# Kernel optimization log

Measured on AMD Instinct MI355X. Metric: run time of the kernel, lower is better.

## Reference

```python
import jax, jax.numpy as jnp
import numpy as np
from jax import lax

B, N, C, T = 8, 2000, 32, 12
K, F_CHEV, F_TIME = 3, 64, 64
LN_EPS = 1e-5


def setup_inputs() -> dict:
    key = jax.random.key(0)
    ks = jax.random.split(key, 20)
    s = 0.1
    return {
        "x": jax.random.normal(ks[0], (B, N, C, T), jnp.float32),
        "cheb_polys": jax.random.normal(ks[1], (K, N, N), jnp.float32) * 0.02,
        # temporal attention params
        "U1": jax.random.normal(ks[2], (N,), jnp.float32) * s,
        "U2": jax.random.normal(ks[3], (C, N), jnp.float32) * s,
        "U3": jax.random.normal(ks[4], (C,), jnp.float32) * s,
        "be": jax.random.normal(ks[5], (1, T, T), jnp.float32) * s,
        "Ve": jax.random.normal(ks[6], (T, T), jnp.float32) * s,
        # spatial attention params
        "W1": jax.random.normal(ks[7], (T,), jnp.float32) * s,
        "W2": jax.random.normal(ks[8], (C, T), jnp.float32) * s,
        "W3": jax.random.normal(ks[9], (C,), jnp.float32) * s,
        "bs": jax.random.normal(ks[10], (1, N, N), jnp.float32) * s,
        "Vs": jax.random.normal(ks[11], (N, N), jnp.float32) * (s / np.sqrt(N)),
        # Chebyshev conv params, stacked (K, C, F_chev)
        "Theta": jax.random.normal(ks[12], (K, C, F_CHEV), jnp.float32) * (1.0 / np.sqrt(C)),
        # time conv (1x3) and residual conv (1x1), NCHW/OIHW layout
        "tc_w": jax.random.normal(ks[13], (F_TIME, F_CHEV, 1, 3), jnp.float32) * (1.0 / np.sqrt(3 * F_CHEV)),
        "tc_b": jnp.zeros((F_TIME,), jnp.float32),
        "rc_w": jax.random.normal(ks[14], (F_TIME, C, 1, 1), jnp.float32) * (1.0 / np.sqrt(C)),
        "rc_b": jnp.zeros((F_TIME,), jnp.float32),
        # LayerNorm over nb_time_filter
        "ln_g": jnp.ones((F_TIME,), jnp.float32),
        "ln_b": jnp.zeros((F_TIME,), jnp.float32),
    }


def _conv2d(x, w, b, stride_t):
    # x: (B, Cin, N, T), w: (Cout, Cin, kh, kw)
    pad_w = (w.shape[3] - 1) // 2
    y = lax.conv_general_dilated(
        x, w, window_strides=(1, stride_t),
        padding=[(0, 0), (pad_w, pad_w)],
        dimension_numbers=("NCHW", "OIHW", "NCHW"))
    return y + b[None, :, None, None]


def reference(x, cheb_polys, U1, U2, U3, be, Ve, W1, W2, W3, bs, Vs,
              Theta, tc_w, tc_b, rc_w, rc_b, ln_g, ln_b):
    b, n, c, t = x.shape

    # ---- temporal attention: (B, T, T) ----
    lhs = jnp.einsum("bnct,n->btc", x, U1)              # x.permute(0,3,2,1) @ U1
    lhs = jnp.einsum("btc,cn->btn", lhs, U2)
    rhs = jnp.einsum("c,bnct->bnt", U3, x)
    E = jnp.einsum("ij,bjk->bik", Ve,
                   jax.nn.sigmoid(jnp.einsum("btn,bnu->btu", lhs, rhs) + be))
    temporal_At = jax.nn.softmax(E, axis=1)             # (B, T, T)

    # apply temporal attention
    x_TAt = jnp.matmul(x.reshape(b, n * c, t), temporal_At).reshape(b, n, c, t)

    # ---- spatial attention on x_TAt: (B, N, N) ----
    lhs_s = jnp.einsum("bnct,t->bnc", x_TAt, W1)
    lhs_s = jnp.einsum("bnc,ct->bnt", lhs_s, W2)
    rhs_s = jnp.einsum("c,bnct->btn", W3, x_TAt)        # (W3 @ x).transpose(-1,-2)
    S = jnp.einsum("ij,bjk->bik", Vs,
                   jax.nn.sigmoid(jnp.einsum("bnt,btm->bnm", lhs_s, rhs_s) + bs))
    spatial_At = jax.nn.softmax(S, axis=1)              # (B, N, N)

    # ---- Chebyshev graph conv with spatial attention ----
    # A[b,k,j,i] = cheb[k,j,i] * SAt[b,j,i]; out = relu(sum_k A^T x Theta_k)
    A = cheb_polys[None, :, :, :] * spatial_At[:, None, :, :]   # (B, K, N, N)
    h = jnp.einsum("bkji,bjct->bkitc", A, x)                    # (B, K, N, T, C)
    spatial_gcn = jax.nn.relu(jnp.einsum("bkitc,kcf->bift", h, Theta))  # (B, N, F, T)

    # ---- temporal conv + residual + LayerNorm ----
    time_out = _conv2d(spatial_gcn.transpose(0, 2, 1, 3), tc_w, tc_b, 1)  # (B, F_time, N, T')
    x_res = _conv2d(x.transpose(0, 2, 1, 3), rc_w, rc_b, 1)               # (B, F_time, N, T')
    z = jax.nn.relu(x_res + time_out).transpose(0, 3, 2, 1)               # (B, T', N, F_time)

    mu = jnp.mean(z, axis=-1, keepdims=True)
    var = jnp.mean((z - mu) ** 2, axis=-1, keepdims=True)
    zn = (z - mu) * lax.rsqrt(var + LN_EPS) * ln_g + ln_b

    return zn.transpose(0, 2, 3, 1)                                       # (B, N, F_time, T')
```

## Files before the change

kernel.cpp:

```cpp
#include <hip/hip_runtime.h>
#include <hip/hip_bf16.h>
#include <math.h>

#define B_ 8
#define N_ 2000
#define C_ 32
#define T_ 12
#define K_ 3
#define FC_ 64
#define FT_ 64
#define PW 2048

typedef short bf16x8 __attribute__((ext_vector_type(8)));
typedef float f32x4 __attribute__((ext_vector_type(4)));

__device__ __forceinline__ float sigmoidf(float v) { return 1.0f / (1.0f + __expf(-v)); }
__device__ __forceinline__ float bf2f(unsigned short u) {
    union { unsigned int i; float f; } v; v.i = ((unsigned int)u) << 16; return v.f;
}
__device__ __forceinline__ unsigned short f2bf(float f) {
    union { __hip_bfloat16 h; unsigned short u; } v; v.h = __float2bfloat16(f); return v.u;
}
typedef const __attribute__((address_space(1))) void* gas_t;
typedef __attribute__((address_space(3))) void* las_t;
__device__ __forceinline__ void gload16(const unsigned short* g, unsigned short* l) {
    __builtin_amdgcn_global_load_lds((gas_t)g, (las_t)l, 16, 0, 0);
}

__global__ __launch_bounds__(256) void k_tprep(const float* __restrict__ x, const float* __restrict__ U1,
                                               const float* __restrict__ U3,
                                               float* __restrict__ rhsT, float* __restrict__ plh) {
    int b = blockIdx.y, chunk = blockIdx.x;
    int tid = threadIdx.x;
    int nl = tid >> 5, c = tid & 31;
    int w = tid >> 6;
    float u3 = U3[c];
    float plA[12];
#pragma unroll
    for (int t = 0; t < 12; ++t) plA[t] = 0.f;
    for (int it = 0; it < 5; ++it) {
        int n = chunk * 40 + it * 8 + nl;
        const float* xp = x + ((size_t)(b * 2000 + n) * 32 + c) * 12;
        float4 v0 = *(const float4*)xp, v1 = *(const float4*)(xp + 4), v2 = *(const float4*)(xp + 8);
        float xv[12] = {v0.x, v0.y, v0.z, v0.w, v1.x, v1.y, v1.z, v1.w, v2.x, v2.y, v2.z, v2.w};
        float rv[12];
#pragma unroll
        for (int t = 0; t < 12; ++t) rv[t] = u3 * xv[t];
#pragma unroll
        for (int off = 16; off >= 1; off >>= 1)
#pragma unroll
            for (int t = 0; t < 12; ++t) rv[t] += __shfl_xor(rv[t], off);
        if (c == 0) {
#pragma unroll
            for (int t = 0; t < 12; ++t) rhsT[(size_t)(b * 2000 + n) * 12 + t] = rv[t];
        }
        float u1 = U1[n];
#pragma unroll
        for (int t = 0; t < 12; ++t) plA[t] += u1 * xv[t];
    }
#pragma unroll
    for (int t = 0; t < 12; ++t) plA[t] += __shfl_xor(plA[t], 32);
    __shared__ float accs[4][32][12];
    if ((tid & 63) < 32) {
#pragma unroll
        for (int t = 0; t < 12; ++t) accs[w][c][t] = plA[t];
    }
    __syncthreads();
    if (tid < 384) {
        int c2 = tid / 12, t2 = tid % 12;
        float s = accs[0][c2][t2] + accs[1][c2][t2] + accs[2][c2][t2] + accs[3][c2][t2];
        plh[((size_t)(b * 50 + chunk)) * 384 + tid] = s;
    }
}

__global__ __launch_bounds__(256) void k_tred(const float* __restrict__ plh, float* __restrict__ lhs1) {
    int b = blockIdx.x;
    for (int q = threadIdx.x; q < 384; q += 256) {
        const float* p = plh + (size_t)b * 50 * 384 + q;
        float s = 0.f;
        for (int ch = 0; ch < 50; ++ch) s += p[(size_t)ch * 384];
        int c = q / 12, t = q % 12;
        lhs1[(b * 12 + t) * 32 + c] = s;
    }
}

__global__ __launch_bounds__(256) void k_lhsT(const float* __restrict__ lhs1, const float* __restrict__ U2,
                                              float* __restrict__ lhsT) {
    int gid = blockIdx.x * 256 + threadIdx.x;
    if (gid >= B_ * T_ * N_) return;
    int n = gid % N_;
    int bt = gid / N_;
    const float* l1 = lhs1 + bt * C_;
    float a = 0.f;
#pragma unroll
    for (int c = 0; c < C_; ++c) a += l1[c] * U2[c * N_ + n];
    lhsT[gid] = a;
}

__global__ __launch_bounds__(256) void k_tatt1(const float* __restrict__ lhsT, const float* __restrict__ rhsT,
                                               float* __restrict__ pP) {
    int b = blockIdx.y, ch = blockIdx.x;
    int tid = threadIdx.x;
    int n0 = ch * 125;
    __shared__ float sL[12][128];
    __shared__ float sR[128][12];
    for (int q = tid; q < 12 * 125; q += 256) {
        int t = q / 125, nn = q % 125;
        sL[t][nn] = lhsT[(size_t)(b * 12 + t) * 2000 + n0 + nn];
    }
    for (int q = tid; q < 125 * 12; q += 256) {
        int nn = q / 12, t = q % 12;
        sR[nn][t] = rhsT[(size_t)(b * 2000 + n0 + nn) * 12 + t];
    }
    __syncthreads();
    if (tid < 144) {
        int tP = tid / 12, uP = tid % 12;
        float a = 0.f;
#pragma unroll 5
        for (int nn = 0; nn < 125; ++nn) a += sL[tP][nn] * sR[nn][uP];
        pP[(size_t)(b * 16 + ch) * 144 + tid] = a;
    }
}

__global__ __launch_bounds__(256) void k_tatt2(const float* __restrict__ pP, const float* __restrict__ be,
                                               const float* __restrict__ Ve, float* __restrict__ At) {
    int b = blockIdx.x, tid = threadIdx.x;
    __shared__ float sp[144], sE[144], mk[12], sk[12];
    int tP = tid / 12, uP = tid % 12;
    if (tid < 144) {
        float a = 0.f;
#pragma unroll
        for (int ch = 0; ch < 16; ++ch) a += pP[(size_t)(b * 16 + ch) * 144 + tid];
        sp[tid] = sigmoidf(a + be[tid]);
    }
    __syncthreads();
    if (tid < 144) {
        float e = 0.f;
#pragma unroll
        for (int j = 0; j < 12; ++j) e += Ve[tP * 12 + j] * sp[j * 12 + uP];
        sE[tid] = e;
    }
    __syncthreads();
    if (tid < 12) {
        float m = -1e30f;
#pragma unroll
        for (int i = 0; i < 12; ++i) m = fmaxf(m, sE[i * 12 + tid]);
        float s = 0.f;
#pragma unroll
        for (int i = 0; i < 12; ++i) s += __expf(sE[i * 12 + tid] - m);
        mk[tid] = m; sk[tid] = 1.0f / s;
    }
    __syncthreads();
    if (tid < 144) At[b * 144 + tid] = __expf(sE[tid] - mk[uP]) * sk[uP];
}

__global__ __launch_bounds__(256) void k_xsp(const float* __restrict__ x, const float* __restrict__ At,
                                             const float* __restrict__ W1, const float* __restrict__ W2,
                                             const float* __restrict__ W3,
                                             float* __restrict__ lhs_s, float* __restrict__ rhs_s) {
    int b = blockIdx.y, chunk = blockIdx.x;
    int tid = threadIdx.x, nl = tid >> 5, c = tid & 31;
    int n = chunk * 8 + nl;
    __shared__ float atl[144];
    __shared__ float w2l[384];
    __shared__ float w1l[12];
    if (tid < 144) atl[tid] = At[b * 144 + tid];
    if (tid >= 144 && tid < 156) w1l[tid - 144] = W1[tid - 144];
    for (int q = tid; q < 384; q += 256) w2l[q] = W2[q];
    __syncthreads();
    const float* xp = x + ((size_t)(b * 2000 + n) * 32 + c) * 12;
    float4 v0 = *(const float4*)xp, v1 = *(const float4*)(xp + 4), v2 = *(const float4*)(xp + 8);
    float xv[12] = {v0.x, v0.y, v0.z, v0.w, v1.x, v1.y, v1.z, v1.w, v2.x, v2.y, v2.z, v2.w};
    float xa[12];
#pragma unroll
    for (int t = 0; t < 12; ++t) {
        float s = 0.f;
#pragma unroll
        for (int u = 0; u < 12; ++u) s += xv[u] * atl[u * 12 + t];
        xa[t] = s;
    }
    float w3 = W3[c];
    float rv[12], lv[12];
    float l1 = 0.f;
#pragma unroll
    for (int t = 0; t < 12; ++t) l1 += xa[t] * w1l[t];
#pragma unroll
    for (int t = 0; t < 12; ++t) { rv[t] = w3 * xa[t]; lv[t] = l1 * w2l[c * 12 + t]; }
#pragma unroll
    for (int off = 16; off >= 1; off >>= 1)
#pragma unroll
        for (int t = 0; t < 12; ++t) { rv[t] += __shfl_xor(rv[t], off); lv[t] += __shfl_xor(lv[t], off); }
    if (c == 0) {
#pragma unroll
        for (int t = 0; t < 12; ++t) rhs_s[(size_t)(b * 12 + t) * 2000 + n] = rv[t];
#pragma unroll
        for (int t = 0; t < 12; ++t) lhs_s[(size_t)(b * 2000 + n) * 12 + t] = lv[t];
    }
}

__global__ __launch_bounds__(256) void k_wprep(const float* __restrict__ tc_w, const float* __restrict__ rc_w,
                                               float* __restrict__ tcwT, float* __restrict__ rcwT) {
    int gid = blockIdx.x * 256 + threadIdx.x;
    if (gid < 12288) {
        int fi = gid / 192, rem = gid % 192, f = rem / 3, d = rem % 3;
        tcwT[gid] = tc_w[(f * 64 + fi) * 3 + d];
    } else if (gid < 14336) {
        int q = gid - 12288;
        int c = q >> 6, f = q & 63;
        rcwT[q] = rc_w[f * 32 + c];
    }
}

__global__ __launch_bounds__(256) void k_vsb(const float* __restrict__ Vs, unsigned short* __restrict__ Vsb) {
    int gid = blockIdx.x * 256 + threadIdx.x;
    int row = gid >> 8, chunk = gid & 255;
    int p0 = chunk * 8;
    unsigned short o[8];
#pragma unroll
    for (int e = 0; e < 8; ++e) {
        int p = p0 + e;
        o[e] = (row < N_ && p < N_) ? f2bf(Vs[row * N_ + p]) : (unsigned short)0;
    }
    *(int4*)(Vsb + (size_t)row * PW + p0) = *(int4*)o;
}

__global__ __launch_bounds__(256) void k_chebT(const float* __restrict__ cheb, unsigned short* __restrict__ chebT) {
    int j0 = blockIdx.x * 64, i0 = blockIdx.y * 64, kk = blockIdx.z;
    __shared__ float Tl[64][65];
    int t = threadIdx.x;
    int rr = t >> 2, c0 = (t & 3) * 16;
    int j = j0 + rr;
#pragma unroll
    for (int e = 0; e < 16; ++e) {
        int i = i0 + c0 + e;
        Tl[rr][c0 + e] = (j < N_ && i < N_) ? cheb[(size_t)kk * 4000000 + (size_t)j * N_ + i] : 0.f;
    }
    __syncthreads();
    int l = t & 63, w = t >> 6;
    unsigned short o[16];
#pragma unroll
    for (int e = 0; e < 16; ++e) o[e] = f2bf(Tl[w * 16 + e][l]);
    unsigned short* dst = chebT + (size_t)kk * PW * PW + (size_t)(i0 + l) * PW + j0 + w * 16;
    *(int4*)dst = *(int4*)o;
    *(int4*)(dst + 8) = *(int4*)(o + 8);
}

__global__ __launch_bounds__(256) void k_xT(const float* __restrict__ x, unsigned short* __restrict__ xT) {
    int j0 = blockIdx.x * 64, r0 = blockIdx.y * 64, b = blockIdx.z;
    __shared__ float Tl[64][65];
    int t = threadIdx.x;
    int rr = t >> 2, c0 = (t & 3) * 16;
    int j = j0 + rr;
#pragma unroll
    for (int e = 0; e < 16; ++e) {
        int r = r0 + c0 + e;
        Tl[rr][c0 + e] = (j < N_) ? x[(size_t)(b * N_ + j) * 384 + r] : 0.f;
    }
    __syncthreads();
    int l = t & 63, w = t >> 6;
    unsigned short o[16];
#pragma unroll
    for (int e = 0; e < 16; ++e) o[e] = f2bf(Tl[w * 16 + e][l]);
    unsigned short* dst = xT + (size_t)b * 384 * PW + (size_t)(r0 + l) * PW + j0 + w * 16;
    *(int4*)dst = *(int4*)o;
    *(int4*)(dst + 8) = *(int4*)(o + 8);
}

__global__ __launch_bounds__(256) void k_sig(const float* __restrict__ lhs_s, const float* __restrict__ rhs_s,
                                             const float* __restrict__ bs, unsigned short* __restrict__ sigT) {
    int p0 = blockIdx.x * 64, i0 = blockIdx.y * 64, b = blockIdx.z;
    __shared__ float sL[64][12];
    __shared__ float sR[12][64];
    __shared__ float bsl[64][65];
    int t = threadIdx.x;
    for (int q = t; q < 768; q += 256) {
        int pp = q / 12, tt = q % 12;
        int p = p0 + pp;
        sL[pp][tt] = (p < N_) ? lhs_s[(b * N_ + p) * 12 + tt] : 0.f;
    }
    for (int q = t; q < 768; q += 256) {
        int tt = q >> 6, ii = q & 63;
        int i = i0 + ii;
        sR[tt][ii] = (i < N_) ? rhs_s[b * (T_ * N_) + tt * N_ + i] : 0.f;
    }
    {
        int pp = t >> 2, c0 = (t & 3) * 16;
        int p = p0 + pp;
        if (p < N_ && i0 + c0 + 15 < N_) {
            const float* src = bs + (size_t)p * N_ + i0 + c0;
#pragma unroll
            for (int e = 0; e < 16; e += 4) *(float4*)&bsl[pp][c0 + e] = *(const float4*)(src + e);
        } else {
#pragma unroll
            for (int e = 0; e < 16; ++e) {
                int i = i0 + c0 + e;
                bsl[pp][c0 + e] = (p < N_ && i < N_) ? bs[(size_t)p * N_ + i] : 0.f;
            }
        }
    }
    __syncthreads();
    int ii = t & 63, w = t >> 6;
    int i = i0 + ii;
    unsigned short o[16];
#pragma unroll
    for (int e = 0; e < 16; ++e) {
        int pl = w * 16 + e;
        int p = p0 + pl;
        float v = 0.f;
        if (p < N_ && i < N_) {
            float d = bsl[pl][ii];
#pragma unroll
            for (int tt = 0; tt < 12; ++tt) d += sL[pl][tt] * sR[tt][ii];
            v = sigmoidf(d);
        }
        o[e] = f2bf(v);
    }
    unsigned short* dst = sigT + (size_t)b * PW * PW + (size_t)i * PW + p0 + w * 16;
    *(int4*)dst = *(int4*)o;
    *(int4*)(dst + 8) = *(int4*)(o + 8);
}

__global__ __launch_bounds__(512) void k_gemm_S_mfma(const unsigned short* __restrict__ Vsb,
                                                     const unsigned short* __restrict__ sigT,
                                                     unsigned short* __restrict__ ST) {
    int lid = blockIdx.x + (blockIdx.y << 3) + (blockIdx.z << 6);
    int swz = (lid & 7) * 64 + (lid >> 3);
    int j0 = (swz & 7) * 256;
    int i0 = ((swz >> 3) & 7) * 256;
    int b = swz >> 6;
    const unsigned short* Ap = sigT + (size_t)b * PW * PW;
    __shared__ unsigned short As[4][8192];
    __shared__ unsigned short Bs[4][8192];
    int t = threadIdx.x, lane = t & 63, w = t >> 6;
    int wr = w >> 2, wc = w & 3;
    f32x4 acc[8][4];
#pragma unroll
    for (int m = 0; m < 8; ++m)
#pragma unroll
        for (int n = 0; n < 4; ++n)
#pragma unroll
            for (int q = 0; q < 4; ++q) acc[m][n][q] = 0.f;
    int srow = t >> 2;
    int sseg = (t & 3) ^ (srow & 3);
    const unsigned short* gA = Ap + (size_t)(i0 + srow) * PW + sseg * 8;
    const unsigned short* gB = Vsb + (size_t)(j0 + srow) * PW + sseg * 8;
    int ldw = w * 512;
#define STG(slot, kt) do { \
    gload16(gA + (size_t)(kt) * 32, &As[slot][ldw]); \
    gload16(gA + (size_t)128 * PW + (size_t)(kt) * 32, &As[slot][4096 + ldw]); \
    gload16(gB + (size_t)(kt) * 32, &Bs[slot][ldw]); \
    gload16(gB + (size_t)128 * PW + (size_t)(kt) * 32, &Bs[slot][4096 + ldw]); \
} while (0)
    STG(0, 0); STG(1, 1); STG(2, 2);
    int l15 = lane & 15;
    int swr = ((lane >> 4) ^ (lane & 3)) * 8;
    int abase = (wr * 128 + l15) * 32 + swr;
    int bbase = (wc * 64 + l15) * 32 + swr;
    for (int kt = 0; kt < 64; ++kt) {
        if (kt < 62)       asm volatile("s_waitcnt vmcnt(8)" ::: "memory");
        else if (kt == 62) asm volatile("s_waitcnt vmcnt(4)" ::: "memory");
        else               asm volatile("s_waitcnt vmcnt(0)" ::: "memory");
        __builtin_amdgcn_s_barrier();
        __builtin_amdgcn_sched_barrier(0);
        if (kt + 3 < 64) STG((kt + 3) & 3, kt + 3);
        int slot = kt & 3;
        bf16x8 af[8], bfv[4];
#pragma unroll
        for (int m = 0; m < 8; ++m) af[m] = *(const bf16x8*)&As[slot][abase + m * 512];
#pragma unroll
        for (int n = 0; n < 4; ++n) bfv[n] = *(const bf16x8*)&Bs[slot][bbase + n * 512];
        __builtin_amdgcn_s_setprio(1);
#pragma unroll
        for (int m = 0; m < 8; ++m)
#pragma unroll
            for (int n = 0; n < 4; ++n)
                acc[m][n] = __builtin_amdgcn_mfma_f32_16x16x32_bf16(af[m], bfv[n], acc[m][n], 0, 0, 0);
        __builtin_amdgcn_s_setprio(0);
    }
#undef STG
    unsigned short* Sp = ST + (size_t)b * PW * PW;
#pragma unroll
    for (int m = 0; m < 8; ++m) {
        int row0 = i0 + wr * 128 + m * 16 + ((lane >> 4) << 2);
#pragma unroll
        for (int n = 0; n < 4; ++n) {
            int col = j0 + wc * 64 + n * 16 + (lane & 15);
#pragma unroll
            for (int q = 0; q < 4; ++q)
                Sp[(size_t)(row0 + q) * PW + col] = f2bf(acc[m][n][q]);
        }
    }
}

__global__ __launch_bounds__(256) void k_smrow(const unsigned short* __restrict__ ST,
                                               float* __restrict__ gm, float* __restrict__ gs) {
    int wid = threadIdx.x >> 6, lane = threadIdx.x & 63;
    int b = blockIdx.y;
    int i = blockIdx.x * 4 + wid;
    const unsigned short* rp = ST + (size_t)b * PW * PW + (size_t)i * PW;
    float vals[32];
    float m = -1e30f;
#pragma unroll
    for (int k = 0; k < 4; ++k) {
        int j0 = lane * 8 + k * 512;
        if (j0 < N_) {
            union { int4 v; unsigned short s[8]; } u;
            u.v = *(const int4*)(rp + j0);
#pragma unroll
            for (int e = 0; e < 8; ++e) {
                vals[k * 8 + e] = bf2f(u.s[e]);
                m = fmaxf(m, vals[k * 8 + e]);
            }
        } else {
#pragma unroll
            for (int e = 0; e < 8; ++e) vals[k * 8 + e] = -1e30f;
        }
    }
#pragma unroll
    for (int off = 32; off >= 1; off >>= 1) m = fmaxf(m, __shfl_xor(m, off));
    float s = 0.f;
#pragma unroll
    for (int k = 0; k < 32; ++k) s += __expf(vals[k] - m);
#pragma unroll
    for (int off = 32; off >= 1; off >>= 1) s += __shfl_xor(s, off);
    if (lane == 0) {
        gm[b * 2048 + i] = m;
        gs[b * 2048 + i] = 1.0f / s;
    }
}

__global__ __launch_bounds__(512) void k_gemm_cheb_mfma(const unsigned short* __restrict__ chebT,
                                                        const unsigned short* __restrict__ ST,
                                                        const float* __restrict__ gm, const float* __restrict__ gs,
                                                        const unsigned short* __restrict__ xT,
                                                        unsigned short* __restrict__ h2) {
    int bk = blockIdx.y;
    int b = bk / 3, kk = bk % 3;
    int i0 = blockIdx.x * 128;
    const unsigned short* Ac = chebT + (size_t)kk * PW * PW;
    const unsigned short* Sa = ST + (size_t)b * PW * PW;
    const unsigned short* Bx = xT + (size_t)b * 384 * PW;
    __shared__ unsigned short As[2][4096];
    __shared__ unsigned short Bs[2][12288];
    int t = threadIdx.x, lane = t & 63, w = t >> 6;
    int wr = w >> 2, wc = w & 3;
    f32x4 acc[4][6];
#pragma unroll
    for (int a = 0; a < 4; ++a)
#pragma unroll
        for (int c = 0; c < 6; ++c)
#pragma unroll
            for (int q = 0; q < 4; ++q) acc[a][c][q] = 0.f;
    int arow = t >> 2, aq = t & 3;
    const unsigned short* gc = Ac + (size_t)(i0 + arow) * PW + aq * 8;
    const unsigned short* gsat = Sa + (size_t)(i0 + arow) * PW + aq * 8;
    float gmv = gm[b * 2048 + i0 + arow];
    float gsv = gs[b * 2048 + i0 + arow];
    int aoff = arow * 32 + (aq ^ (arow & 3)) * 8;
    int bseg = (t & 3) ^ ((t >> 2) & 3);
    const unsigned short* gB = Bx + (size_t)(t >> 2) * PW + bseg * 8;
    int ldso = w * 512;
#define STAGE_B(buf, p) do { \
    gload16(gB + (p), &Bs[buf][ldso]); \
    gload16(gB + 128 * PW + (p), &Bs[buf][4096 + ldso]); \
    gload16(gB + 256 * PW + (p), &Bs[buf][8192 + ldso]); \
} while (0)
    union U8 { int4 v; unsigned short s[8]; };
    U8 ca, sa;
    ca.v = *(const int4*)gc;
    sa.v = *(const int4*)gsat;
    STAGE_B(0, 0);
    {
        U8 o;
#pragma unroll
        for (int e = 0; e < 8; ++e) o.s[e] = f2bf(bf2f(ca.s[e]) * __expf(bf2f(sa.s[e]) - gmv) * gsv);
        *(int4*)&As[0][aoff] = o.v;
    }
    ca.v = *(const int4*)(gc + 32);
    sa.v = *(const int4*)(gsat + 32);
    __syncthreads();
    int cur = 0;
    int rswz = ((lane >> 4) ^ (lane & 3)) * 8;
    for (int p = 0; p < PW; p += 32) {
        if (p + 32 < PW) {
            STAGE_B(cur ^ 1, p + 32);
            U8 o;
#pragma unroll
            for (int e = 0; e < 8; ++e) o.s[e] = f2bf(bf2f(ca.s[e]) * __expf(bf2f(sa.s[e]) - gmv) * gsv);
            *(int4*)&As[cur ^ 1][aoff] = o.v;
            int pn = (p + 64 < PW) ? p + 64 : 0;
            ca.v = *(const int4*)(gc + pn);
            sa.v = *(const int4*)(gsat + pn);
        }
        bf16x8 af[4], bfr[6];
#pragma unroll
        for (int fm = 0; fm < 4; ++fm)
            af[fm] = *(const bf16x8*)&As[cur][(wr * 64 + fm * 16 + (lane & 15)) * 32 + rswz];
#pragma unroll
        for (int fn = 0; fn < 6; ++fn)
            bfr[fn] = *(const bf16x8*)&Bs[cur][(wc * 96 + fn * 16 + (lane & 15)) * 32 + rswz];
#pragma unroll
        for (int fm = 0; fm < 4; ++fm)
#pragma unroll
            for (int fn = 0; fn < 6; ++fn)
                acc[fm][fn] = __builtin_amdgcn_mfma_f32_16x16x32_bf16(af[fm], bfr[fn], acc[fm][fn], 0, 0, 0);
        __syncthreads();
        cur ^= 1;
    }
#undef STAGE_B
    unsigned short* hp = h2 + (size_t)bk * 768000;
#pragma unroll
    for (int fm = 0; fm < 4; ++fm) {
        int row0 = i0 + wr * 64 + fm * 16 + ((lane >> 4) << 2);
#pragma unroll
        for (int fn = 0; fn < 6; ++fn) {
            int col = wc * 96 + fn * 16 + (lane & 15);
#pragma unroll
            for (int q = 0; q < 4; ++q) {
                int row = row0 + q;
                if (row < N_) hp[(size_t)row * 384 + col] = f2bf(acc[fm][fn][q]);
            }
        }
    }
}

__global__ __launch_bounds__(512) void k_final3(const float* __restrict__ x, const unsigned short* __restrict__ h2,
                                                const float* __restrict__ ThetaG,
                                                const float* __restrict__ tcwT, const float* __restrict__ tc_b,
                                                const float* __restrict__ rcwT, const float* __restrict__ rc_b,
                                                const float* __restrict__ ln_g, const float* __restrict__ ln_b,
                                                float* __restrict__ out) {
    __shared__ __align__(16) char smem[110848];
    unsigned int* gl = (unsigned int*)smem;
    unsigned short* th = (unsigned short*)(smem + 98560);
    float* red_s = (float*)(smem + 98560);
    float* red_q = red_s + 64 * 13;

    int tid = threadIdx.x;
    int n_l = tid & 63, fg = tid >> 6;
    int b = blockIdx.y;
    int node = blockIdx.x * 64 + n_l;
    bool ok = node < N_;
    int nd = ok ? node : N_ - 1;

    for (int q = tid; q < 6144; q += 512) th[q] = f2bf(ThetaG[q]);
    __syncthreads();

    float acc[8][12];
#pragma unroll
    for (int ff = 0; ff < 8; ++ff)
#pragma unroll
        for (int t = 0; t < 12; ++t) acc[ff][t] = 0.f;
    const unsigned short* hb = h2 + (size_t)b * 3 * 768000 + (size_t)nd * 384;
#pragma unroll
    for (int kk = 0; kk < 3; ++kk) {
        const unsigned short* hp = hb + (size_t)kk * 768000;
#pragma unroll 2
        for (int c = 0; c < 32; ++c) {
            const unsigned short* hq = hp + c * 12;
            uint2 u0 = *(const uint2*)(hq);
            uint2 u1 = *(const uint2*)(hq + 4);
            uint2 u2 = *(const uint2*)(hq + 8);
            float h[12];
            h[0] = bf2f((unsigned short)u0.x);  h[1] = bf2f((unsigned short)(u0.x >> 16));
            h[2] = bf2f((unsigned short)u0.y);  h[3] = bf2f((unsigned short)(u0.y >> 16));
            h[4] = bf2f((unsigned short)u1.x);  h[5] = bf2f((unsigned short)(u1.x >> 16));
            h[6] = bf2f((unsigned short)u1.y);  h[7] = bf2f((unsigned short)(u1.y >> 16));
            h[8] = bf2f((unsigned short)u2.x);  h[9] = bf2f((unsigned short)(u2.x >> 16));
            h[10] = bf2f((unsigned short)u2.y); h[11] = bf2f((unsigned short)(u2.y >> 16));
            const unsigned short* wv = th + (kk * 32 + c) * 64 + fg * 8;
            uint2 w01 = *(const uint2*)wv;
            uint2 w23 = *(const uint2*)(wv + 4);
            float wf[8];
            wf[0] = bf2f((unsigned short)w01.x); wf[1] = bf2f((unsigned short)(w01.x >> 16));
            wf[2] = bf2f((unsigned short)w01.y); wf[3] = bf2f((unsigned short)(w01.y >> 16));
            wf[4] = bf2f((unsigned short)w23.x); wf[5] = bf2f((unsigned short)(w23.x >> 16));
            wf[6] = bf2f((unsigned short)w23.y); wf[7] = bf2f((unsigned short)(w23.y >> 16));
#pragma unroll
            for (int ff = 0; ff < 8; ++ff)
#pragma unroll
                for (int t = 0; t < 12; ++t) acc[ff][t] = fmaf(h[t], wf[ff], acc[ff][t]);
        }
    }
    unsigned int* gr = gl + n_l * 385 + fg * 48;
#pragma unroll
    for (int ff = 0; ff < 8; ++ff)
#pragma unroll
        for (int tp = 0; tp < 6; ++tp) {
            float a0 = fmaxf(acc[ff][2 * tp], 0.f), a1 = fmaxf(acc[ff][2 * tp + 1], 0.f);
            gr[ff * 6 + tp] = (unsigned int)f2bf(a0) | ((unsigned int)f2bf(a1) << 16);
        }
    __syncthreads();

    float z[8][12];
#pragma unroll
    for (int ff = 0; ff < 8; ++ff) {
        float bias = tc_b[fg * 8 + ff] + rc_b[fg * 8 + ff];
#pragma unroll
        for (int t = 0; t < 12; ++t) z[ff][t] = bias;
    }
    const float* xp = x + (size_t)(b * 2000 + nd) * 384;
#pragma unroll 2
    for (int c = 0; c < 32; ++c) {
        float4 x0 = *(const float4*)(xp + c * 12);
        float4 x1 = *(const float4*)(xp + c * 12 + 4);
        float4 x2 = *(const float4*)(xp + c * 12 + 8);
        float xv[12] = {x0.x, x0.y, x0.z, x0.w, x1.x, x1.y, x1.z, x1.w, x2.x, x2.y, x2.z, x2.w};
        float4 r0 = *(const float4*)(rcwT + c * 64 + fg * 8);
        float4 r1 = *(const float4*)(rcwT + c * 64 + fg * 8 + 4);
        float rw[8] = {r0.x, r0.y, r0.z, r0.w, r1.x, r1.y, r1.z, r1.w};
#pragma unroll
        for (int ff = 0; ff < 8; ++ff)
#pragma unroll
            for (int t = 0; t < 12; ++t) z[ff][t] = fmaf(xv[t], rw[ff], z[ff][t]);
    }
    const unsigned int* grow = gl + n_l * 385;
    for (int fi = 0; fi < 64; ++fi) {
        float g[12];
#pragma unroll
        for (int j = 0; j < 6; ++j) {
            unsigned int u = grow[fi * 6 + j];
            g[2 * j] = bf2f((unsigned short)u);
            g[2 * j + 1] = bf2f((unsigned short)(u >> 16));
        }
        const float* wp = tcwT + (fi * 64 + fg * 8) * 3;
        float4 w0 = *(const float4*)(wp);
        float4 w1 = *(const float4*)(wp + 4);
        float4 w2 = *(const float4*)(wp + 8);
        float4 w3 = *(const float4*)(wp + 12);
        float4 w4 = *(const float4*)(wp + 16);
        float4 w5 = *(const float4*)(wp + 20);
        float wb[24] = {w0.x, w0.y, w0.z, w0.w, w1.x, w1.y, w1.z, w1.w,
                        w2.x, w2.y, w2.z, w2.w, w3.x, w3.y, w3.z, w3.w,
                        w4.x, w4.y, w4.z, w4.w, w5.x, w5.y, w5.z, w5.w};
#pragma unroll
        for (int ff = 0; ff < 8; ++ff) {
            float a0 = wb[ff * 3], a1 = wb[ff * 3 + 1], a2 = wb[ff * 3 + 2];
            z[ff][0] = fmaf(g[0], a1, fmaf(g[1], a2, z[ff][0]));
#pragma unroll
            for (int t = 1; t < 11; ++t)
                z[ff][t] = fmaf(g[t - 1], a0, fmaf(g[t], a1, fmaf(g[t + 1], a2, z[ff][t])));
            z[ff][11] = fmaf(g[10], a0, fmaf(g[11], a1, z[ff][11]));
        }
    }
#pragma unroll
    for (int ff = 0; ff < 8; ++ff)
#pragma unroll
        for (int t = 0; t < 12; ++t) z[ff][t] = fmaxf(z[ff][t], 0.f);

    float s[12], q[12];
#pragma unroll
    for (int t = 0; t < 12; ++t) { s[t] = 0.f; q[t] = 0.f; }
#pragma unroll
    for (int ff = 0; ff < 8; ++ff)
#pragma unroll
        for (int t = 0; t < 12; ++t) { s[t] += z[ff][t]; q[t] += z[ff][t] * z[ff][t]; }
    __syncthreads();
    for (int g = 0; g < 8; ++g) {
        if (fg == g) {
            if (g == 0) {
#pragma unroll
                for (int t = 0; t < 12; ++t) { red_s[n_l * 13 + t] = s[t]; red_q[n_l * 13 + t] = q[t]; }
            } else {
#pragma unroll
                for (int t = 0; t < 12; ++t) { red_s[n_l * 13 + t] += s[t]; red_q[n_l * 13 + t] += q[t]; }
            }
        }
        __syncthreads();
    }
    float mu[12], rs[12];
#pragma unroll
    for (int t = 0; t < 12; ++t) {
        float m = red_s[n_l * 13 + t] * (1.0f / 64.0f);
        float v = red_q[n_l * 13 + t] * (1.0f / 64.0f) - m * m;
        mu[t] = m;
        rs[t] = rsqrtf(v + 1e-5f);
    }
    if (ok) {
        float* op = out + ((size_t)(b * 2000 + node) * 64 + fg * 8) * 12;
#pragma unroll
        for (int ff = 0; ff < 8; ++ff) {
            float lg = ln_g[fg * 8 + ff], lb = ln_b[fg * 8 + ff];
            float o[12];
#pragma unroll
            for (int t = 0; t < 12; ++t) o[t] = (z[ff][t] - mu[t]) * rs[t] * lg + lb;
#pragma unroll
            for (int tq = 0; tq < 3; ++tq)
                *(float4*)(op + ff * 12 + tq * 4) = make_float4(o[tq * 4], o[tq * 4 + 1], o[tq * 4 + 2], o[tq * 4 + 3]);
        }
    }
}

extern "C" void kernel_launch(void* const* d_in, const int* in_sizes, int n_in,
                              void* d_out, int out_size, void* d_ws, size_t ws_size,
                              hipStream_t stream) {
    const float* x     = (const float*)d_in[0];
    const float* cheb  = (const float*)d_in[1];
    const float* U1    = (const float*)d_in[2];
    const float* U2    = (const float*)d_in[3];
    const float* U3    = (const float*)d_in[4];
    const float* be    = (const float*)d_in[5];
    const float* Ve    = (const float*)d_in[6];
    const float* W1    = (const float*)d_in[7];
    const float* W2    = (const float*)d_in[8];
    const float* W3    = (const float*)d_in[9];
    const float* bs    = (const float*)d_in[10];
    const float* Vs    = (const float*)d_in[11];
    const float* Theta = (const float*)d_in[12];
    const float* tc_w  = (const float*)d_in[13];
    const float* tc_b  = (const float*)d_in[14];
    const float* rc_w  = (const float*)d_in[15];
    const float* rc_b  = (const float*)d_in[16];
    const float* ln_g  = (const float*)d_in[17];
    const float* ln_b  = (const float*)d_in[18];
    float* out = (float*)d_out;

    float* ws    = (float*)d_ws;
    float* At    = ws;
    float* lhs1  = ws + 1152;
    float* lhsT  = ws + 4224;
    float* rhsT  = ws + 196224;
    float* lhs_s = ws + 388224;
    float* rhs_s = ws + 580224;
    float* gm    = ws + 772224;
    float* gs    = ws + 788608;
    float* tcwT  = ws + 804992;
    float* rcwT  = ws + 817280;
    float* plh   = ws + 819328;
    float* pP    = ws + 972928;
    unsigned short* Vsb   = (unsigned short*)(ws + 991360);
    unsigned short* chebT = (unsigned short*)(ws + 3088512);
    unsigned short* xT    = (unsigned short*)(ws + 9379968);
    unsigned short* sigT  = (unsigned short*)(ws + 12525696);
    unsigned short* h2    = sigT;
    unsigned short* STb   = (unsigned short*)(ws + 29302912);

    k_wprep<<<56, 256, 0, stream>>>(tc_w, rc_w, tcwT, rcwT);
    k_vsb<<<2048, 256, 0, stream>>>(Vs, Vsb);
    k_chebT<<<dim3(32, 32, 3), 256, 0, stream>>>(cheb, chebT);
    k_xT<<<dim3(32, 6, 8), 256, 0, stream>>>(x, xT);
    k_tprep<<<dim3(50, 8), 256, 0, stream>>>(x, U1, U3, rhsT, plh);
    k_tred<<<8, 256, 0, stream>>>(plh, lhs1);
    k_lhsT<<<750, 256, 0, stream>>>(lhs1, U2, lhsT);
    k_tatt1<<<dim3(16, 8), 256, 0, stream>>>(lhsT, rhsT, pP);
    k_tatt2<<<8, 256, 0, stream>>>(pP, be, Ve, At);
    k_xsp<<<dim3(250, 8), 256, 0, stream>>>(x, At, W1, W2, W3, lhs_s, rhs_s);
    k_sig<<<dim3(32, 32, 8), 256, 0, stream>>>(lhs_s, rhs_s, bs, sigT);
    k_gemm_S_mfma<<<dim3(8, 8, 8), 512, 0, stream>>>(Vsb, sigT, STb);
    k_smrow<<<dim3(512, 8), 256, 0, stream>>>(STb, gm, gs);
    k_gemm_cheb_mfma<<<dim3(16, 24), 512, 0, stream>>>(chebT, STb, gm, gs, xT, h2);
    k_final3<<<dim3(32, 8), 512, 0, stream>>>(x, h2, Theta, tcwT, tc_b, rcwT, rc_b, ln_g, ln_b, out);
}
```

Baseline: 645.4 us.

## Restructure S GEMM into double-buffered K=64 tiles with quadrant-split MFMA phases

The Vs·sigmoid GEMM moves from a 4-slot K=32 ring to a 2-slot K=64 double buffer with an 8-way XOR swizzle. Each K tile is split into four quadrant phases, and the next tile's A and B loads are issued between phases. This is meant to interleave LDS reads, global prefetch and MFMA more finely, and to halve the number of outer iterations. In exchange it adds three extra barriers per iteration, a full vmcnt(0) wait at the top of each iteration, and a shallower prefetch depth.

```diff
diff --git a/kernel.cpp b/kernel.cpp
--- a/kernel.cpp
+++ b/kernel.cpp
@@ -329,10 +329,11 @@
     int i0 = ((swz >> 3) & 7) * 256;
     int b = swz >> 6;
     const unsigned short* Ap = sigT + (size_t)b * PW * PW;
-    __shared__ unsigned short As[4][8192];
-    __shared__ unsigned short Bs[4][8192];
+    __shared__ unsigned short As[2][16384];
+    __shared__ unsigned short Bs[2][16384];
     int t = threadIdx.x, lane = t & 63, w = t >> 6;
     int wr = w >> 2, wc = w & 3;
+    int l15 = lane & 15, kseg = lane >> 4;
     f32x4 acc[8][4];
 #pragma unroll
     for (int m = 0; m < 8; ++m)
@@ -340,54 +341,81 @@
         for (int n = 0; n < 4; ++n)
 #pragma unroll
             for (int q = 0; q < 4; ++q) acc[m][n][q] = 0.f;
-    int srow = t >> 2;
-    int sseg = (t & 3) ^ (srow & 3);
-    const unsigned short* gA = Ap + (size_t)(i0 + srow) * PW + sseg * 8;
-    const unsigned short* gB = Vsb + (size_t)(j0 + srow) * PW + sseg * 8;
+    int srow = t >> 3;
+    int schunk = ((t & 7) ^ (srow & 7)) * 8;
+    const unsigned short* gA = Ap + (size_t)(i0 + srow) * PW + schunk;
+    const unsigned short* gB = Vsb + (size_t)(j0 + srow) * PW + schunk;
     int ldw = w * 512;
-#define STG(slot, kt) do { \
-    gload16(gA + (size_t)(kt) * 32, &As[slot][ldw]); \
-    gload16(gA + (size_t)128 * PW + (size_t)(kt) * 32, &As[slot][4096 + ldw]); \
-    gload16(gB + (size_t)(kt) * 32, &Bs[slot][ldw]); \
-    gload16(gB + (size_t)128 * PW + (size_t)(kt) * 32, &Bs[slot][4096 + ldw]); \
+#define SA_(buf_, kt_, h_) do { \
+    gload16(gA + (size_t)((h_) * 128) * PW + (kt_) * 64, &As[buf_][(h_) * 8192 + ldw]); \
+    gload16(gA + (size_t)((h_) * 128 + 64) * PW + (kt_) * 64, &As[buf_][(h_) * 8192 + 4096 + ldw]); \
 } while (0)
-    STG(0, 0); STG(1, 1); STG(2, 2);
-    int l15 = lane & 15;
-    int swr = ((lane >> 4) ^ (lane & 3)) * 8;
-    int abase = (wr * 128 + l15) * 32 + swr;
-    int bbase = (wc * 64 + l15) * 32 + swr;
-    for (int kt = 0; kt < 64; ++kt) {
-        if (kt < 62)       asm volatile("s_waitcnt vmcnt(8)" ::: "memory");
-        else if (kt == 62) asm volatile("s_waitcnt vmcnt(4)" ::: "memory");
-        else               asm volatile("s_waitcnt vmcnt(0)" ::: "memory");
+#define SB_(buf_, kt_, h_) do { \
+    gload16(gB + (size_t)((h_) * 128) * PW + (kt_) * 64, &Bs[buf_][(h_) * 8192 + ldw]); \
+    gload16(gB + (size_t)((h_) * 128 + 64) * PW + (kt_) * 64, &Bs[buf_][(h_) * 8192 + 4096 + ldw]); \
+} while (0)
+#define RDA(dst, mh_, buf_) do { \
+    _Pragma("unroll") for (int m = 0; m < 4; ++m) { \
+        int R = wr * 128 + (mh_) * 64 + m * 16 + l15; \
+        _Pragma("unroll") for (int kh = 0; kh < 2; ++kh) \
+            dst[m][kh] = *(const bf16x8*)&As[buf_][R * 64 + (((kh * 4 + kseg) ^ (R & 7)) << 3)]; \
+    } } while (0)
+#define RDB(dst, nh_, buf_) do { \
+    _Pragma("unroll") for (int n = 0; n < 2; ++n) { \
+        int R = wc * 64 + (nh_) * 32 + n * 16 + l15; \
+        _Pragma("unroll") for (int kh = 0; kh < 2; ++kh) \
+            dst[n][kh] = *(const bf16x8*)&Bs[buf_][R * 64 + (((kh * 4 + kseg) ^ (R & 7)) << 3)]; \
+    } } while (0)
+#define LGKM0 do { asm volatile("s_waitcnt lgkmcnt(0)" ::: "memory"); __builtin_amdgcn_sched_barrier(0); } while (0)
+#define MMA(av, bv, mh_, nh_) do { \
+    __builtin_amdgcn_s_setprio(1); \
+    _Pragma("unroll") for (int m = 0; m < 4; ++m) \
+    _Pragma("unroll") for (int n = 0; n < 2; ++n) \
+    _Pragma("unroll") for (int kh = 0; kh < 2; ++kh) \
+        acc[m + (mh_) * 4][n + (nh_) * 2] = __builtin_amdgcn_mfma_f32_16x16x32_bf16( \
+            av[m][kh], bv[n][kh], acc[m + (mh_) * 4][n + (nh_) * 2], 0, 0, 0); \
+    __builtin_amdgcn_s_setprio(0); } while (0)
+    SA_(0, 0, 0); SA_(0, 0, 1); SB_(0, 0, 0); SB_(0, 0, 1);
+    for (int kt = 0; kt < 32; ++kt) {
+        int buf = kt & 1, nbuf = buf ^ 1;
+        bf16x8 aR[4][2], bR[2][2];
+        asm volatile("s_waitcnt vmcnt(0)" ::: "memory");
         __builtin_amdgcn_s_barrier();
         __builtin_amdgcn_sched_barrier(0);
-        if (kt + 3 < 64) STG((kt + 3) & 3, kt + 3);
-        int slot = kt & 3;
-        bf16x8 af[8], bfv[4];
-#pragma unroll
-        for (int m = 0; m < 8; ++m) af[m] = *(const bf16x8*)&As[slot][abase + m * 512];
-#pragma unroll
-        for (int n = 0; n < 4; ++n) bfv[n] = *(const bf16x8*)&Bs[slot][bbase + n * 512];
-        __builtin_amdgcn_s_setprio(1);
-#pragma unroll
-        for (int m = 0; m < 8; ++m)
-#pragma unroll
-            for (int n = 0; n < 4; ++n)
-                acc[m][n] = __builtin_amdgcn_mfma_f32_16x16x32_bf16(af[m], bfv[n], acc[m][n], 0, 0, 0);
-        __builtin_amdgcn_s_setprio(0);
-    }
-#undef STG
+        if (kt + 1 < 32) { SA_(nbuf, kt + 1, 0); SA_(nbuf, kt + 1, 1); }
+        RDA(aR, 0, buf); RDB(bR, 0, buf);
+        LGKM0;
+        MMA(aR, bR, 0, 0);
+        __builtin_amdgcn_s_barrier();
+        if (kt + 1 < 32) { SB_(nbuf, kt + 1, 0); SB_(nbuf, kt + 1, 1); }
+        RDB(bR, 1, buf);
+        LGKM0;
+        MMA(aR, bR, 0, 1);
+        __builtin_amdgcn_s_barrier();
+        RDA(aR, 1, buf); RDB(bR, 0, buf);
+        LGKM0;
+        MMA(aR, bR, 1, 0);
+        __builtin_amdgcn_s_barrier();
+        RDB(bR, 1, buf);
+        LGKM0;
+        MMA(aR, bR, 1, 1);
+    }
+#undef SA_
+#undef SB_
+#undef RDA
+#undef RDB
+#undef LGKM0
+#undef MMA
     unsigned short* Sp = ST + (size_t)b * PW * PW;
 #pragma unroll
-    for (int m = 0; m < 8; ++m) {
-        int row0 = i0 + wr * 128 + m * 16 + ((lane >> 4) << 2);
-#pragma unroll
-        for (int n = 0; n < 4; ++n) {
-            int col = j0 + wc * 64 + n * 16 + (lane & 15);
+    for (int mi = 0; mi < 8; ++mi) {
+        int row0 = i0 + wr * 128 + (mi >> 2) * 64 + (mi & 3) * 16 + (kseg << 2);
+#pragma unroll
+        for (int ni = 0; ni < 4; ++ni) {
+            int col = j0 + wc * 64 + (ni >> 1) * 32 + (ni & 1) * 16 + l15;
 #pragma unroll
             for (int q = 0; q < 4; ++q)
-                Sp[(size_t)(row0 + q) * PW + col] = f2bf(acc[m][n][q]);
+                Sp[(size_t)(row0 + q) * PW + col] = f2bf(acc[mi][ni][q]);
         }
     }
 }
```

Result: no change. 637.4 us (-1.2%).
